# Kernel optimization log

Measured on AMD Instinct MI355X. Metric: run time of the kernel, lower is better.

## Reference

```python
import jax, jax.numpy as jnp
import numpy as np

N = 100000   # nodes
E = 3200000  # directed edges
F_IN = 128   # data.num_node_features
H = 16       # hidden
C = 2        # output classes (hard-coded in module)


def _glorot(key, fan_in, fan_out):
    s = jnp.sqrt(6.0 / (fan_in + fan_out)).astype(jnp.float32)
    return jax.random.uniform(key, (fan_in, fan_out), jnp.float32, -s, s)


def setup_inputs() -> dict:
    key = jax.random.key(0)
    ks = jax.random.split(key, 5)
    x = jax.random.normal(ks[0], (N, F_IN), jnp.float32)
    edge_index = jax.random.randint(ks[1], (2, E), 0, N, dtype=jnp.int64)
    return {
        "x": x,
        "edge_index": edge_index,
        "W1": _glorot(ks[2], F_IN, H), "b1": jnp.zeros((H,), jnp.float32),
        "W2": _glorot(ks[3], H, H),    "b2": jnp.zeros((H,), jnp.float32),
        "W3": _glorot(ks[4], H, C),    "b3": jnp.zeros((C,), jnp.float32),
    }


def _gcn_conv(x, W, b, src, dst, norm, n):
    # PyG GCNConv: linear transform, then normalized gather -> scatter-add, + bias
    h = x @ W                                   # [N, out]
    msg = h[src] * norm[:, None]                # [E+N, out] gather over source nodes
    out = jax.ops.segment_sum(msg, dst, num_segments=n)  # scatter-add at targets
    return out + b


def reference(x, edge_index, W1, b1, W2, b2, W3, b3):
    n = x.shape[0]
    loop = jnp.arange(n, dtype=edge_index.dtype)
    src = jnp.concatenate([edge_index[0], loop])  # add self-loops (PyG default)
    dst = jnp.concatenate([edge_index[1], loop])
    # symmetric normalization: deg^{-1/2}[src] * deg^{-1/2}[dst], deg = in-degree w/ self-loops
    deg = jax.ops.segment_sum(jnp.ones(src.shape, jnp.float32), dst, num_segments=n)
    dis = jnp.where(deg > 0, jax.lax.rsqrt(jnp.maximum(deg, 1.0)), 0.0)
    norm = dis[src] * dis[dst]
    # dropout is identity in eval mode
    h = jax.nn.relu(_gcn_conv(x, W1, b1, src, dst, norm, n))
    h = jax.nn.relu(_gcn_conv(h, W2, b2, src, dst, norm, n))
    h = _gcn_conv(h, W3, b3, src, dst, norm, n)
    return jax.nn.log_softmax(h, axis=1)
```

## Files before the change

### kernel.cpp

```cpp
#include <hip/hip_runtime.h>
#include <math.h>

#define NSB   512
#define BSH   8
#define BKN   256
#define ESMAX 6272
#define SLOT  10240

typedef _Float16 h8  __attribute__((ext_vector_type(8)));
typedef _Float16 h4  __attribute__((ext_vector_type(4)));
typedef _Float16 h2v __attribute__((ext_vector_type(2)));

__device__ inline int wave_scan_incl(int v) {
    int lane = threadIdx.x & 63;
#pragma unroll
    for (int d = 1; d < 64; d <<= 1) {
        int t = __shfl_up(v, d, 64);
        if (lane >= d) v += t;
    }
    return v;
}


union BU {
    struct {
        unsigned sorted[ESMAX];
        int lc[512], lofE[512], lcur[512], soff[512];
        int wsum[8];
        unsigned char sbuck[ESMAX];
    } b;
    struct { float sW[2048]; } l;
};

__global__ __launch_bounds__(512) void k_build(
        const int* __restrict__ srcv, const int* __restrict__ dstv,
        const float* __restrict__ x, const float* __restrict__ W1,
        int* __restrict__ gcur, unsigned* __restrict__ col,
        _Float16* __restrict__ hsRaw,
        int e, int nbuck, int es, int n, int nlin) {
    __shared__ BU su;
    int tid = threadIdx.x;

    if (blockIdx.x < NSB) {
        su.b.lc[tid] = 0;
        __syncthreads();
        int lo = blockIdx.x * es;
        int hi = min(lo + es, e);
        for (int i = lo + tid; i < hi; i += 512)
            atomicAdd(&su.b.lc[dstv[i] >> BSH], 1);
        __syncthreads();
        int c = su.b.lc[tid];
        int inc = wave_scan_incl(c);
        int wid = tid >> 6;
        if ((tid & 63) == 63) su.b.wsum[wid] = inc;
        __syncthreads();
        int wofs = 0;
#pragma unroll
        for (int w = 0; w < 8; w++) wofs += (w < wid) ? su.b.wsum[w] : 0;
        int excl = inc - c + wofs;
        su.b.lofE[tid] = excl;
        su.b.lcur[tid] = excl;
        if (tid < nbuck && c > 0)
            su.b.soff[tid] = tid * SLOT + atomicAdd(&gcur[tid], c);
        __syncthreads();
        for (int i = lo + tid; i < hi; i += 512) {
            int d = dstv[i];
            int bb = d >> BSH;
            int p = atomicAdd(&su.b.lcur[bb], 1);
            su.b.sorted[p] = ((unsigned)srcv[i] << BSH) | (unsigned)(d & (BKN - 1));
            su.b.sbuck[p] = (unsigned char)(bb & 255);
        }
        __syncthreads();
        int cnt_ = hi - lo;
        int split = (nbuck > 256) ? su.b.lofE[256] : 0x7fffffff;
        for (int i = tid; i < cnt_; i += 512) {
            int bb = su.b.sbuck[i] | ((i >= split) ? 256 : 0);
            col[su.b.soff[bb] + (i - su.b.lofE[bb])] = su.b.sorted[i];
        }
    } else {
        for (int i = tid; i < 2048; i += 512) su.l.sW[i] = W1[i];
        __syncthreads();
        int cgi = tid & 3;
        int kg  = (tid >> 2) & 15;
        int wv  = tid >> 6;
        float wr[8][4];
#pragma unroll
        for (int j = 0; j < 8; j++)
#pragma unroll
            for (int cc = 0; cc < 4; cc++)
                wr[j][cc] = su.l.sW[(kg * 8 + j) * 16 + cgi * 4 + cc];
        int lb = blockIdx.x - NSB;
        for (int base = lb * 8; base < n; base += nlin * 8) {
            int node = base + wv;
            float a0 = 0.f, a1 = 0.f, a2 = 0.f, a3 = 0.f;
            if (node < n) {
                const float4* xr = (const float4*)(x + (size_t)node * 128 + kg * 8);
                float4 xv0 = xr[0], xv1 = xr[1];
                float xs[8] = {xv0.x, xv0.y, xv0.z, xv0.w, xv1.x, xv1.y, xv1.z, xv1.w};
#pragma unroll
                for (int j = 0; j < 8; j++) {
                    a0 += xs[j] * wr[j][0];
                    a1 += xs[j] * wr[j][1];
                    a2 += xs[j] * wr[j][2];
                    a3 += xs[j] * wr[j][3];
                }
            }
#pragma unroll
            for (int m = 4; m <= 32; m <<= 1) {
                a0 += __shfl_xor(a0, m);
                a1 += __shfl_xor(a1, m);
                a2 += __shfl_xor(a2, m);
                a3 += __shfl_xor(a3, m);
            }
            if (kg == 0 && node < n) {
                h4 o;
                o[0] = (_Float16)a0;
                o[1] = (_Float16)a1;
                o[2] = (_Float16)a2;
                o[3] = (_Float16)a3;
                *((h4*)(hsRaw + (size_t)node * 16 + cgi * 4)) = o;
            }
        }
    }
}


__global__ __launch_bounds__(512) void k_sort2(
        const unsigned* __restrict__ col, const int* __restrict__ gcur,
        int* __restrict__ col2, int* __restrict__ rs,
        int* __restrict__ re, float* __restrict__ dis,
        const _Float16* __restrict__ hsRaw, _Float16* __restrict__ hsA, int n) {
    __shared__ int cnt[BKN];
    __shared__ int cur[BKN];
    __shared__ int wsum[4];
    __shared__ float sdis[BKN];
    int tid = threadIdx.x;
    int bk = blockIdx.x;
    int lo = bk * SLOT;
    int hi = lo + gcur[bk];
    if (tid < BKN) cnt[tid] = 0;
    __syncthreads();
    for (int i = lo + tid; i < hi; i += 512)
        atomicAdd(&cnt[col[i] & (BKN - 1u)], 1);
    __syncthreads();
    int c = (tid < BKN) ? cnt[tid] : 0;
    int inc = wave_scan_incl(c);
    int wid = tid >> 6;
    if (tid < BKN && (tid & 63) == 63) wsum[wid] = inc;
    __syncthreads();
    if (tid < BKN) {
        int wofs = 0;
#pragma unroll
        for (int w = 0; w < 4; w++) wofs += (w < wid) ? wsum[w] : 0;
        int excl = inc - c + wofs;
        cur[tid] = lo + excl;
        float d = rsqrtf((float)(c + 1));
        sdis[tid] = d;
        int node = (bk << BSH) + tid;
        if (node < n) {
            rs[node] = lo + excl;
            re[node] = lo + excl + c;
            dis[node] = d;
        }
    }
    __syncthreads();
    for (int i = lo + tid; i < hi; i += 512) {
        unsigned v = col[i];
        int pos = atomicAdd(&cur[v & (BKN - 1u)], 1);
        col2[pos] = (int)(v >> BSH);
    }
    {
        int node = (bk << BSH) + (tid >> 1);
        if (node < n) {
            float d = sdis[tid >> 1];
            h8 v = ((const h8*)hsRaw)[(size_t)node * 2 + (tid & 1)];
            h8 o;
#pragma unroll
            for (int j = 0; j < 8; j++) o[j] = (_Float16)((float)v[j] * d);
            ((h8*)hsA)[(size_t)node * 2 + (tid & 1)] = o;
        }
    }
}


__global__ __launch_bounds__(256) void k_pullA(
        const _Float16* __restrict__ hs, const int* __restrict__ rs,
        const int* __restrict__ re, const int* __restrict__ col2,
        const float* __restrict__ dis, const float* __restrict__ bb,
        const float* __restrict__ W, _Float16* __restrict__ hsOut, int n) {
    __shared__ float sW[256];
    __shared__ float sb[16];
    if (threadIdx.x < 256) sW[threadIdx.x] = W[threadIdx.x];
    if (threadIdx.x < 16) sb[threadIdx.x] = bb[threadIdx.x];
    __syncthreads();
    long long t = (long long)blockIdx.x * blockDim.x + threadIdx.x;
    int node = (int)(t >> 2), qt = (int)(t & 3);
    if (node >= n) return;
    const h8* H = (const h8*)hs;
    float acc[16];
    if (qt == 0) {
        h8 s0 = H[(size_t)node * 2];
        h8 s1 = H[(size_t)node * 2 + 1];
#pragma unroll
        for (int j = 0; j < 8; j++) { acc[j] = (float)s0[j]; acc[8 + j] = (float)s1[j]; }
    } else {
#pragma unroll
        for (int j = 0; j < 16; j++) acc[j] = 0.f;
    }
    int b = rs[node], e2 = re[node];
    int i = b + qt;
    for (; i + 12 < e2; i += 16) {
        int s0 = col2[i], s1 = col2[i + 4], s2 = col2[i + 8], s3 = col2[i + 12];
        h8 a0 = H[(size_t)s0 * 2], b0 = H[(size_t)s0 * 2 + 1];
        h8 a1 = H[(size_t)s1 * 2], b1 = H[(size_t)s1 * 2 + 1];
        h8 a2 = H[(size_t)s2 * 2], b2 = H[(size_t)s2 * 2 + 1];
        h8 a3 = H[(size_t)s3 * 2], b3 = H[(size_t)s3 * 2 + 1];
#pragma unroll
        for (int j = 0; j < 8; j++) {
            acc[j]     += (float)a0[j] + (float)a1[j] + (float)a2[j] + (float)a3[j];
            acc[8 + j] += (float)b0[j] + (float)b1[j] + (float)b2[j] + (float)b3[j];
        }
    }
    for (; i < e2; i += 4) {
        int s = col2[i];
        h8 a = H[(size_t)s * 2], bq = H[(size_t)s * 2 + 1];
#pragma unroll
        for (int j = 0; j < 8; j++) { acc[j] += (float)a[j]; acc[8 + j] += (float)bq[j]; }
    }
#pragma unroll
    for (int j = 0; j < 16; j++) {
        acc[j] += __shfl_xor(acc[j], 1);
        acc[j] += __shfl_xor(acc[j], 2);
    }
    float d = dis[node];
    float va[16];
#pragma unroll
    for (int k = 0; k < 16; k++) {
        float v = acc[k] * d + sb[k];
        va[k] = v > 0.f ? v : 0.f;
    }
    h4 o;
#pragma unroll
    for (int cc = 0; cc < 4; cc++) {
        int cidx = (qt << 2) + cc;
        float s = 0.f;
#pragma unroll
        for (int k = 0; k < 16; k++) s += va[k] * sW[k * 16 + cidx];
        o[cc] = (_Float16)(s * d);
    }
    *((h4*)(hsOut + (size_t)node * 16 + (qt << 2))) = o;
}


__global__ __launch_bounds__(256) void k_pullB(
        const _Float16* __restrict__ hs, const int* __restrict__ rs,
        const int* __restrict__ re, const int* __restrict__ col2,
        const float* __restrict__ dis, const float* __restrict__ bb,
        const float* __restrict__ W, _Float16* __restrict__ hs2, int n) {
    __shared__ float sW[32];
    __shared__ float sb[16];
    if (threadIdx.x < 32) sW[threadIdx.x] = W[threadIdx.x];
    if (threadIdx.x < 16) sb[threadIdx.x] = bb[threadIdx.x];
    __syncthreads();
    long long t = (long long)blockIdx.x * blockDim.x + threadIdx.x;
    int node = (int)(t >> 2), qt = (int)(t & 3);
    if (node >= n) return;
    const h8* H = (const h8*)hs;
    float acc[16];
    if (qt == 0) {
        h8 s0 = H[(size_t)node * 2];
        h8 s1 = H[(size_t)node * 2 + 1];
#pragma unroll
        for (int j = 0; j < 8; j++) { acc[j] = (float)s0[j]; acc[8 + j] = (float)s1[j]; }
    } else {
#pragma unroll
        for (int j = 0; j < 16; j++) acc[j] = 0.f;
    }
    int b = rs[node], e2 = re[node];
    int i = b + qt;
    for (; i + 12 < e2; i += 16) {
        int s0 = col2[i], s1 = col2[i + 4], s2 = col2[i + 8], s3 = col2[i + 12];
        h8 a0 = H[(size_t)s0 * 2], b0 = H[(size_t)s0 * 2 + 1];
        h8 a1 = H[(size_t)s1 * 2], b1 = H[(size_t)s1 * 2 + 1];
        h8 a2 = H[(size_t)s2 * 2], b2 = H[(size_t)s2 * 2 + 1];
        h8 a3 = H[(size_t)s3 * 2], b3 = H[(size_t)s3 * 2 + 1];
#pragma unroll
        for (int j = 0; j < 8; j++) {
            acc[j]     += (float)a0[j] + (float)a1[j] + (float)a2[j] + (float)a3[j];
            acc[8 + j] += (float)b0[j] + (float)b1[j] + (float)b2[j] + (float)b3[j];
        }
    }
    for (; i < e2; i += 4) {
        int s = col2[i];
        h8 a = H[(size_t)s * 2], bq = H[(size_t)s * 2 + 1];
#pragma unroll
        for (int j = 0; j < 8; j++) { acc[j] += (float)a[j]; acc[8 + j] += (float)bq[j]; }
    }
#pragma unroll
    for (int j = 0; j < 16; j++) {
        acc[j] += __shfl_xor(acc[j], 1);
        acc[j] += __shfl_xor(acc[j], 2);
    }
    float d = dis[node];
    float p0 = 0.f, p1 = 0.f;
#pragma unroll
    for (int k = 0; k < 16; k++) {
        float v = acc[k] * d + sb[k];
        v = v > 0.f ? v : 0.f;
        p0 += v * sW[k * 2 + 0];
        p1 += v * sW[k * 2 + 1];
    }
    if (qt == 0) {
        h2v o;
        o[0] = (_Float16)(p0 * d);
        o[1] = (_Float16)(p1 * d);
        ((h2v*)hs2)[node] = o;
    }
}


__global__ __launch_bounds__(256) void k_pull2lsm(
        const _Float16* __restrict__ hs2, const int* __restrict__ rs,
        const int* __restrict__ re, const int* __restrict__ col2,
        const float* __restrict__ dis, const float* __restrict__ b3,
        float* __restrict__ out, int n) {
    long long t = (long long)blockIdx.x * blockDim.x + threadIdx.x;
    int node = (int)(t >> 2), qt = (int)(t & 3);
    if (node >= n) return;
    const h2v* H = (const h2v*)hs2;
    float a0 = 0.f, a1 = 0.f;
    if (qt == 0) {
        h2v self = H[node];
        a0 = (float)self[0]; a1 = (float)self[1];
    }
    int b = rs[node], e2 = re[node];
    int i = b + qt;
    for (; i + 12 < e2; i += 16) {
        h2v v0 = H[col2[i]];
        h2v v1 = H[col2[i + 4]];
        h2v v2 = H[col2[i + 8]];
        h2v v3 = H[col2[i + 12]];
        a0 += (float)v0[0] + (float)v1[0] + (float)v2[0] + (float)v3[0];
        a1 += (float)v0[1] + (float)v1[1] + (float)v2[1] + (float)v3[1];
    }
    for (; i < e2; i += 4) {
        h2v v = H[col2[i]];
        a0 += (float)v[0];
        a1 += (float)v[1];
    }
    a0 += __shfl_xor(a0, 1); a0 += __shfl_xor(a0, 2);
    a1 += __shfl_xor(a1, 1); a1 += __shfl_xor(a1, 2);
    if (qt == 0) {
        float d = dis[node];
        float z0 = a0 * d + b3[0];
        float z1 = a1 * d + b3[1];
        float m = fmaxf(z0, z1);
        float l = m + logf(expf(z0 - m) + expf(z1 - m));
        float2 o = {z0 - l, z1 - l};
        ((float2*)out)[node] = o;
    }
}


extern "C" void kernel_launch(void* const* d_in, const int* in_sizes, int n_in,
                              void* d_out, int out_size, void* d_ws, size_t ws_size,
                              hipStream_t stream) {
    const float* x  = (const float*)d_in[0];
    const int*   ei = (const int*)d_in[1];
    const float* W1 = (const float*)d_in[2];
    const float* b1 = (const float*)d_in[3];
    const float* W2 = (const float*)d_in[4];
    const float* b2 = (const float*)d_in[5];
    const float* W3 = (const float*)d_in[6];
    const float* b3 = (const float*)d_in[7];
    float* out = (float*)d_out;

    const int N = in_sizes[0] / 128;
    const int E = in_sizes[1] / 2;
    const int* src = ei;
    const int* dst = ei + E;

    const int NBUCK = (N + BKN - 1) >> BSH;
    const int ES = (E + NSB - 1) / NSB;
    const int NLIN = (N + 127) / 128;

    char* ws = (char*)d_ws;
    size_t off = 0;
    auto alloc = [&](size_t bytes) {
        void* p = ws + off;
        off += (bytes + 255) & ~(size_t)255;
        return p;
    };
    int*       gcur  = (int*)alloc((size_t)NBUCK * sizeof(int));
    unsigned*  col   = (unsigned*)alloc((size_t)NBUCK * SLOT * sizeof(unsigned));
    int*       col2  = (int*)alloc((size_t)NBUCK * SLOT * sizeof(int));
    int*       rs    = (int*)alloc((size_t)N * sizeof(int));
    int*       re    = (int*)alloc((size_t)N * sizeof(int));
    float*     dis   = (float*)alloc((size_t)N * sizeof(float));
    _Float16*  hsRaw = (_Float16*)alloc((size_t)N * 16 * sizeof(_Float16));
    _Float16*  hsA   = (_Float16*)alloc((size_t)N * 16 * sizeof(_Float16));
    _Float16*  hsB   = (_Float16*)alloc((size_t)N * 16 * sizeof(_Float16));
    _Float16*  hs2   = (_Float16*)alloc((size_t)N * 2 * sizeof(_Float16));

    const int B = 256;
    auto g = [&](long long work) { return (int)((work + B - 1) / B); };

    hipMemsetAsync(gcur, 0, (size_t)NBUCK * sizeof(int), stream);

    k_build<<<NSB + NLIN, 512, 0, stream>>>(src, dst, x, W1, gcur, col, hsRaw,
                                            E, NBUCK, ES, N, NLIN);

    k_sort2<<<NBUCK, 512, 0, stream>>>(col, gcur, col2, rs, re, dis, hsRaw, hsA, N);

    k_pullA<<<g((long long)N * 4), B, 0, stream>>>(hsA, rs, re, col2, dis, b1, W2, hsB, N);

    k_pullB<<<g((long long)N * 4), B, 0, stream>>>(hsB, rs, re, col2, dis, b2, W3, hs2, N);

    k_pull2lsm<<<g((long long)N * 4), B, 0, stream>>>(hs2, rs, re, col2, dis, b3, out, N);
}
```

Measured before the change: 261.1 us.

## Move first-layer linear into sort kernel and apply source norm in pull

```diff
diff --git a/kernel.cpp b/kernel.cpp
--- a/kernel.cpp
+++ b/kernel.cpp
@@ -1,10 +1,10 @@
 #include <hip/hip_runtime.h>
 #include <math.h>
 
-#define NSB   512
+#define NSB   1024
 #define BSH   8
 #define BKN   256
-#define ESMAX 6272
+#define ESMAX 3136
 #define SLOT  10240
 
 typedef _Float16 h8  __attribute__((ext_vector_type(8)));
@@ -22,60 +22,100 @@
 }
 
 
-union BU {
-    struct {
-        unsigned sorted[ESMAX];
-        int lc[512], lofE[512], lcur[512], soff[512];
-        int wsum[8];
-        unsigned char sbuck[ESMAX];
-    } b;
+__global__ __launch_bounds__(512) void k_bucket(
+        const int* __restrict__ src, const int* __restrict__ dst,
+        int* __restrict__ gcur, unsigned* __restrict__ col,
+        int e, int nbuck, int es) {
+    __shared__ unsigned sorted[ESMAX];
+    __shared__ unsigned char sbuck[ESMAX];
+    __shared__ int lc[512], lofE[512], lcur[512], soff[512];
+    __shared__ int wsum[8];
+    int tid = threadIdx.x;
+    lc[tid] = 0;
+    __syncthreads();
+    int lo = blockIdx.x * es;
+    int hi = min(lo + es, e);
+    for (int i = lo + tid; i < hi; i += 512)
+        atomicAdd(&lc[dst[i] >> BSH], 1);
+    __syncthreads();
+    int c = lc[tid];
+    int inc = wave_scan_incl(c);
+    int wid = tid >> 6;
+    if ((tid & 63) == 63) wsum[wid] = inc;
+    __syncthreads();
+    int wofs = 0;
+#pragma unroll
+    for (int w = 0; w < 8; w++) wofs += (w < wid) ? wsum[w] : 0;
+    int excl = inc - c + wofs;
+    lofE[tid] = excl;
+    lcur[tid] = excl;
+    if (tid < nbuck && c > 0)
+        soff[tid] = tid * SLOT + atomicAdd(&gcur[tid], c);
+    __syncthreads();
+    for (int i = lo + tid; i < hi; i += 512) {
+        int d = dst[i];
+        int b = d >> BSH;
+        int p = atomicAdd(&lcur[b], 1);
+        sorted[p] = ((unsigned)src[i] << BSH) | (unsigned)(d & (BKN - 1));
+        sbuck[p] = (unsigned char)(b & 255);
+    }
+    __syncthreads();
+    int cnt_ = hi - lo;
+    int split = (nbuck > 256) ? lofE[256] : 0x7fffffff;
+    for (int i = tid; i < cnt_; i += 512) {
+        int b = sbuck[i] | ((i >= split) ? 256 : 0);
+        col[soff[b] + (i - lofE[b])] = sorted[i];
+    }
+}
+
+
+union SLU {
+    struct { int cnt[BKN], cur[BKN], wsum[4]; } s;
     struct { float sW[2048]; } l;
 };
 
-__global__ __launch_bounds__(512) void k_build(
-        const int* __restrict__ srcv, const int* __restrict__ dstv,
+__global__ __launch_bounds__(512) void k_sortlin(
+        const unsigned* __restrict__ col, const int* __restrict__ gcur,
+        int* __restrict__ col2, int* __restrict__ rs,
+        int* __restrict__ re, float* __restrict__ dis,
         const float* __restrict__ x, const float* __restrict__ W1,
-        int* __restrict__ gcur, unsigned* __restrict__ col,
         _Float16* __restrict__ hsRaw,
-        int e, int nbuck, int es, int n, int nlin) {
-    __shared__ BU su;
+        int n, int nbuck, int nlin) {
+    __shared__ SLU su;
     int tid = threadIdx.x;
 
-    if (blockIdx.x < NSB) {
-        su.b.lc[tid] = 0;
+    if ((int)blockIdx.x < nbuck) {
+        int bk = blockIdx.x;
+        int lo = bk * SLOT;
+        int hi = lo + gcur[bk];
+        if (tid < BKN) su.s.cnt[tid] = 0;
         __syncthreads();
-        int lo = blockIdx.x * es;
-        int hi = min(lo + es, e);
         for (int i = lo + tid; i < hi; i += 512)
-            atomicAdd(&su.b.lc[dstv[i] >> BSH], 1);
+            atomicAdd(&su.s.cnt[col[i] & (BKN - 1u)], 1);
         __syncthreads();
-        int c = su.b.lc[tid];
+        int c = (tid < BKN) ? su.s.cnt[tid] : 0;
         int inc = wave_scan_incl(c);
         int wid = tid >> 6;
-        if ((tid & 63) == 63) su.b.wsum[wid] = inc;
+        if (tid < BKN && (tid & 63) == 63) su.s.wsum[wid] = inc;
         __syncthreads();
-        int wofs = 0;
-#pragma unroll
-        for (int w = 0; w < 8; w++) wofs += (w < wid) ? su.b.wsum[w] : 0;
-        int excl = inc - c + wofs;
-        su.b.lofE[tid] = excl;
-        su.b.lcur[tid] = excl;
-        if (tid < nbuck && c > 0)
-            su.b.soff[tid] = tid * SLOT + atomicAdd(&gcur[tid], c);
+        if (tid < BKN) {
+            int wofs = 0;
+#pragma unroll
+            for (int w = 0; w < 4; w++) wofs += (w < wid) ? su.s.wsum[w] : 0;
+            int excl = inc - c + wofs;
+            su.s.cur[tid] = lo + excl;
+            int node = (bk << BSH) + tid;
+            if (node < n) {
+                rs[node] = lo + excl;
+                re[node] = lo + excl + c;
+                dis[node] = rsqrtf((float)(c + 1));
+            }
+        }
         __syncthreads();
         for (int i = lo + tid; i < hi; i += 512) {
-            int d = dstv[i];
-            int bb = d >> BSH;
-            int p = atomicAdd(&su.b.lcur[bb], 1);
-            su.b.sorted[p] = ((unsigned)srcv[i] << BSH) | (unsigned)(d & (BKN - 1));
-            su.b.sbuck[p] = (unsigned char)(bb & 255);
-        }
-        __syncthreads();
-        int cnt_ = hi - lo;
-        int split = (nbuck > 256) ? su.b.lofE[256] : 0x7fffffff;
-        for (int i = tid; i < cnt_; i += 512) {
-            int bb = su.b.sbuck[i] | ((i >= split) ? 256 : 0);
-            col[su.b.soff[bb] + (i - su.b.lofE[bb])] = su.b.sorted[i];
+            unsigned v = col[i];
+            int pos = atomicAdd(&su.s.cur[v & (BKN - 1u)], 1);
+            col2[pos] = (int)(v >> BSH);
         }
     } else {
         for (int i = tid; i < 2048; i += 512) su.l.sW[i] = W1[i];
@@ -89,7 +129,7 @@
 #pragma unroll
             for (int cc = 0; cc < 4; cc++)
                 wr[j][cc] = su.l.sW[(kg * 8 + j) * 16 + cgi * 4 + cc];
-        int lb = blockIdx.x - NSB;
+        int lb = blockIdx.x - nbuck;
         for (int base = lb * 8; base < n; base += nlin * 8) {
             int node = base + wv;
             float a0 = 0.f, a1 = 0.f, a2 = 0.f, a3 = 0.f;
@@ -125,65 +165,7 @@
 }
 
 
-__global__ __launch_bounds__(512) void k_sort2(
-        const unsigned* __restrict__ col, const int* __restrict__ gcur,
-        int* __restrict__ col2, int* __restrict__ rs,
-        int* __restrict__ re, float* __restrict__ dis,
-        const _Float16* __restrict__ hsRaw, _Float16* __restrict__ hsA, int n) {
-    __shared__ int cnt[BKN];
-    __shared__ int cur[BKN];
-    __shared__ int wsum[4];
-    __shared__ float sdis[BKN];
-    int tid = threadIdx.x;
-    int bk = blockIdx.x;
-    int lo = bk * SLOT;
-    int hi = lo + gcur[bk];
-    if (tid < BKN) cnt[tid] = 0;
-    __syncthreads();
-    for (int i = lo + tid; i < hi; i += 512)
-        atomicAdd(&cnt[col[i] & (BKN - 1u)], 1);
-    __syncthreads();
-    int c = (tid < BKN) ? cnt[tid] : 0;
-    int inc = wave_scan_incl(c);
-    int wid = tid >> 6;
-    if (tid < BKN && (tid & 63) == 63) wsum[wid] = inc;
-    __syncthreads();
-    if (tid < BKN) {
-        int wofs = 0;
-#pragma unroll
-        for (int w = 0; w < 4; w++) wofs += (w < wid) ? wsum[w] : 0;
-        int excl = inc - c + wofs;
-        cur[tid] = lo + excl;
-        float d = rsqrtf((float)(c + 1));
-        sdis[tid] = d;
-        int node = (bk << BSH) + tid;
-        if (node < n) {
-            rs[node] = lo + excl;
-            re[node] = lo + excl + c;
-            dis[node] = d;
-        }
-    }
-    __syncthreads();
-    for (int i = lo + tid; i < hi; i += 512) {
-        unsigned v = col[i];
-        int pos = atomicAdd(&cur[v & (BKN - 1u)], 1);
-        col2[pos] = (int)(v >> BSH);
-    }
-    {
-        int node = (bk << BSH) + (tid >> 1);
-        if (node < n) {
-            float d = sdis[tid >> 1];
-            h8 v = ((const h8*)hsRaw)[(size_t)node * 2 + (tid & 1)];
-            h8 o;
-#pragma unroll
-            for (int j = 0; j < 8; j++) o[j] = (_Float16)((float)v[j] * d);
-            ((h8*)hsA)[(size_t)node * 2 + (tid & 1)] = o;
-        }
-    }
-}
-
-
-__global__ __launch_bounds__(256) void k_pullA(
+__global__ __launch_bounds__(256) void k_pullA2(
         const _Float16* __restrict__ hs, const int* __restrict__ rs,
         const int* __restrict__ re, const int* __restrict__ col2,
         const float* __restrict__ dis, const float* __restrict__ bb,
@@ -197,12 +179,13 @@
     int node = (int)(t >> 2), qt = (int)(t & 3);
     if (node >= n) return;
     const h8* H = (const h8*)hs;
+    float d = dis[node];
     float acc[16];
     if (qt == 0) {
         h8 s0 = H[(size_t)node * 2];
         h8 s1 = H[(size_t)node * 2 + 1];
 #pragma unroll
-        for (int j = 0; j < 8; j++) { acc[j] = (float)s0[j]; acc[8 + j] = (float)s1[j]; }
+        for (int j = 0; j < 8; j++) { acc[j] = (float)s0[j] * d; acc[8 + j] = (float)s1[j] * d; }
     } else {
 #pragma unroll
         for (int j = 0; j < 16; j++) acc[j] = 0.f;
@@ -211,28 +194,29 @@
     int i = b + qt;
     for (; i + 12 < e2; i += 16) {
         int s0 = col2[i], s1 = col2[i + 4], s2 = col2[i + 8], s3 = col2[i + 12];
+        float d0 = dis[s0], d1 = dis[s1], d2 = dis[s2], d3 = dis[s3];
         h8 a0 = H[(size_t)s0 * 2], b0 = H[(size_t)s0 * 2 + 1];
         h8 a1 = H[(size_t)s1 * 2], b1 = H[(size_t)s1 * 2 + 1];
         h8 a2 = H[(size_t)s2 * 2], b2 = H[(size_t)s2 * 2 + 1];
         h8 a3 = H[(size_t)s3 * 2], b3 = H[(size_t)s3 * 2 + 1];
 #pragma unroll
         for (int j = 0; j < 8; j++) {
-            acc[j]     += (float)a0[j] + (float)a1[j] + (float)a2[j] + (float)a3[j];
-            acc[8 + j] += (float)b0[j] + (float)b1[j] + (float)b2[j] + (float)b3[j];
+            acc[j]     += (float)a0[j] * d0 + (float)a1[j] * d1 + (float)a2[j] * d2 + (float)a3[j] * d3;
+            acc[8 + j] += (float)b0[j] * d0 + (float)b1[j] * d1 + (float)b2[j] * d2 + (float)b3[j] * d3;
         }
     }
     for (; i < e2; i += 4) {
         int s = col2[i];
+        float ds = dis[s];
         h8 a = H[(size_t)s * 2], bq = H[(size_t)s * 2 + 1];
 #pragma unroll
-        for (int j = 0; j < 8; j++) { acc[j] += (float)a[j]; acc[8 + j] += (float)bq[j]; }
+        for (int j = 0; j < 8; j++) { acc[j] += (float)a[j] * ds; acc[8 + j] += (float)bq[j] * ds; }
     }
 #pragma unroll
     for (int j = 0; j < 16; j++) {
         acc[j] += __shfl_xor(acc[j], 1);
         acc[j] += __shfl_xor(acc[j], 2);
     }
-    float d = dis[node];
     float va[16];
 #pragma unroll
     for (int k = 0; k < 16; k++) {
@@ -381,7 +365,8 @@
     const int* dst = ei + E;
 
     const int NBUCK = (N + BKN - 1) >> BSH;
-    const int ES = (E + NSB - 1) / NSB;
+    int ES = (E + NSB - 1) / NSB;
+    if (ES > ESMAX) ES = ESMAX;
     const int NLIN = (N + 127) / 128;
 
     char* ws = (char*)d_ws;
@@ -398,7 +383,6 @@
     int*       re    = (int*)alloc((size_t)N * sizeof(int));
     float*     dis   = (float*)alloc((size_t)N * sizeof(float));
     _Float16*  hsRaw = (_Float16*)alloc((size_t)N * 16 * sizeof(_Float16));
-    _Float16*  hsA   = (_Float16*)alloc((size_t)N * 16 * sizeof(_Float16));
     _Float16*  hsB   = (_Float16*)alloc((size_t)N * 16 * sizeof(_Float16));
     _Float16*  hs2   = (_Float16*)alloc((size_t)N * 2 * sizeof(_Float16));
 
@@ -407,12 +391,12 @@
 
     hipMemsetAsync(gcur, 0, (size_t)NBUCK * sizeof(int), stream);
 
-    k_build<<<NSB + NLIN, 512, 0, stream>>>(src, dst, x, W1, gcur, col, hsRaw,
-                                            E, NBUCK, ES, N, NLIN);
-
-    k_sort2<<<NBUCK, 512, 0, stream>>>(col, gcur, col2, rs, re, dis, hsRaw, hsA, N);
-
-    k_pullA<<<g((long long)N * 4), B, 0, stream>>>(hsA, rs, re, col2, dis, b1, W2, hsB, N);
+    k_bucket<<<NSB, 512, 0, stream>>>(src, dst, gcur, col, E, NBUCK, ES);
+
+    k_sortlin<<<NBUCK + NLIN, 512, 0, stream>>>(col, gcur, col2, rs, re, dis,
+                                                x, W1, hsRaw, N, NBUCK, NLIN);
+
+    k_pullA2<<<g((long long)N * 4), B, 0, stream>>>(hsRaw, rs, re, col2, dis, b1, W2, hsB, N);
 
     k_pullB<<<g((long long)N * 4), B, 0, stream>>>(hsB, rs, re, col2, dis, b2, W3, hs2, N);
 
```

Measured after the change: 276.7 us. 6.0% more time.
